# Kernel tuning notes

Hardware: AMD Instinct MI355X
Metric: run time of the kernel (lower is better)

## Reference

```python
import jax, jax.numpy as jnp
import numpy as np

N, E, DIN, DH, DE, DOUT, G = 100000, 1600000, 64, 128, 16, 1, 256

def setup_inputs() -> dict:
    key = jax.random.key(0)
    ks = jax.random.split(key, 16)
    p = lambda k, s: (jax.random.normal(k, s, dtype=jnp.float32) * 0.05)
    return {
        "x": jax.random.normal(ks[0], (N, DIN), dtype=jnp.float32),
        "edge_index": jax.random.randint(ks[1], (2, E), 0, N, dtype=jnp.int64),
        "edge_attr": jax.random.normal(ks[2], (E, DE), dtype=jnp.float32),
        "batch": jnp.sort(jax.random.randint(ks[3], (N,), 0, G, dtype=jnp.int64)),
        # GINEConv 1: edge lin (edge_dim -> input_dim) + mlp1 (DIN->DH->DH)
        "ew1": p(ks[4], (DIN, DE)), "eb1": p(ks[5], (DIN,)),
        "w1a": p(ks[6], (DH, DIN)), "b1a": p(ks[7], (DH,)),
        "w1b": p(ks[8], (DH, DH)), "b1b": p(ks[9], (DH,)),
        # GINEConv 2: edge lin (edge_dim -> hidden_dim) + mlp2 (DH->DH->DH)
        "ew2": p(ks[10], (DH, DE)), "eb2": p(ks[11], (DH,)),
        "w2a": p(ks[12], (DH, DH)), "b2a": p(ks[13], (DH,)),
        "w2b": p(ks[14], (DH, DH)), "b2b": p(ks[15], (DH,)),
        "wf": p(jax.random.fold_in(key, 99), (DOUT, DH)),
        "bf": jnp.zeros((DOUT,), dtype=jnp.float32),
    }

def _gine(x, src, dst, edge_attr, ew, eb, wa, ba, wb, bb):
    # message = relu(x[src] + Lin(edge_attr)); sum-aggregate at dst; eps=0
    msg = jax.nn.relu(x[src] + edge_attr @ ew.T + eb)          # [E, D]
    aggr = jax.ops.segment_sum(msg, dst, num_segments=x.shape[0])
    h = x + aggr                                               # (1+eps)*x + aggr, eps=0
    h = jax.nn.relu(h @ wa.T + ba)
    return h @ wb.T + bb

def reference(x, edge_index, edge_attr, batch, ew1, eb1, w1a, b1a, w1b, b1b,
              ew2, eb2, w2a, b2a, w2b, b2b, wf, bf):
    src, dst = edge_index[0], edge_index[1]
    h = _gine(x, src, dst, edge_attr, ew1, eb1, w1a, b1a, w1b, b1b)
    h = jax.nn.relu(h)  # dropout is identity in eval mode
    h = _gine(h, src, dst, edge_attr, ew2, eb2, w2a, b2a, w2b, b2b)
    h = jax.nn.relu(h)
    # global mean pool over graphs
    sums = jax.ops.segment_sum(h, batch, num_segments=G)       # [G, DH]
    cnts = jax.ops.segment_sum(jnp.ones((h.shape[0],), h.dtype), batch, num_segments=G)
    pooled = sums / jnp.maximum(cnts, 1.0)[:, None]
    return pooled @ wf.T + bf                                  # [G, DOUT]
```

## Files before the change

### kernel.cpp

```cpp
#include <hip/hip_runtime.h>

#define DINc 64
#define DHc  128
#define DEc  16
#define Gc   256
#define Rrep 64
#define SCB  1024

typedef unsigned short u16;
typedef unsigned int   u32;
typedef __attribute__((ext_vector_type(8))) short bf8;
typedef __attribute__((ext_vector_type(4))) short bf4;
typedef __attribute__((ext_vector_type(4))) float f4;

__device__ __forceinline__ u16 f2b(float f) {
  u32 u = __builtin_bit_cast(u32, f);
  u32 r = u + 0x7FFFu + ((u >> 16) & 1u);
  return (u16)(r >> 16);
}
__device__ __forceinline__ float b2f(u16 h) {
  u32 u = ((u32)h) << 16;
  return __builtin_bit_cast(float, u);
}

__global__ __launch_bounds__(256) void k_cvt(const float* __restrict__ x,
                                             u16* __restrict__ xb, const int n8) {
  for (int i = blockIdx.x * 256 + threadIdx.x; i < n8; i += gridDim.x * 256) {
    float4 f0 = *(const float4*)(x + (size_t)i * 8);
    float4 f1 = *(const float4*)(x + (size_t)i * 8 + 4);
    bf8 v;
    v[0]=(short)f2b(f0.x); v[1]=(short)f2b(f0.y); v[2]=(short)f2b(f0.z); v[3]=(short)f2b(f0.w);
    v[4]=(short)f2b(f1.x); v[5]=(short)f2b(f1.y); v[6]=(short)f2b(f1.z); v[7]=(short)f2b(f1.w);
    *(bf8*)(xb + (size_t)i * 8) = v;
  }
}

__global__ __launch_bounds__(256) void k_hist(const int* __restrict__ dstA, const int nE,
                                              int* __restrict__ deg) {
  for (int i = blockIdx.x * 256 + threadIdx.x; i < nE; i += gridDim.x * 256)
    atomicAdd(&deg[dstA[i]], 1);
}

__global__ __launch_bounds__(256) void k_scan_blk(const int* __restrict__ deg,
                                                  int* __restrict__ bsum, const int nN) {
  const int b = blockIdx.x, t = threadIdx.x;
  const int i0 = b * SCB + t * 4;
  int s = 0;
  #pragma unroll
  for (int q = 0; q < 4; ++q) { const int i = i0 + q; if (i < nN) s += deg[i]; }
  #pragma unroll
  for (int off = 32; off > 0; off >>= 1) s += __shfl_down(s, off);
  __shared__ int ws[4];
  if ((t & 63) == 0) ws[t >> 6] = s;
  __syncthreads();
  if (t == 0) bsum[b] = ws[0] + ws[1] + ws[2] + ws[3];
}

__global__ __launch_bounds__(256) void k_scan_fin(const int* __restrict__ deg,
                                                  const int* __restrict__ bsum,
                                                  int* __restrict__ rowptr,
                                                  const int nN, const int nB) {
  const int b = blockIdx.x, t = threadIdx.x;
  int p = 0;
  for (int i = t; i < b; i += 256) p += bsum[i];
  #pragma unroll
  for (int off = 32; off > 0; off >>= 1) p += __shfl_down(p, off);
  __shared__ int ws[4];
  __shared__ int sc[256];
  if ((t & 63) == 0) ws[t >> 6] = p;
  const int i0 = b * SCB + t * 4;
  int vals[4]; int s = 0;
  #pragma unroll
  for (int q = 0; q < 4; ++q) { const int i = i0 + q; vals[q] = (i < nN) ? deg[i] : 0; s += vals[q]; }
  sc[t] = s;
  __syncthreads();
  const int boff = ws[0] + ws[1] + ws[2] + ws[3];
  for (int off = 1; off < 256; off <<= 1) {
    int u = (t >= off) ? sc[t - off] : 0;
    __syncthreads();
    sc[t] += u;
    __syncthreads();
  }
  int run = boff + sc[t] - s;
  #pragma unroll
  for (int q = 0; q < 4; ++q) { const int i = i0 + q; if (i < nN) rowptr[i] = run; run += vals[q]; }
  if (b == nB - 1 && t == 255) rowptr[nN] = run;
}

__global__ __launch_bounds__(256) void k_fill(const int* __restrict__ dstA,
                                              const int* __restrict__ srcA, const int nE,
                                              const int* __restrict__ rowptr,
                                              int* __restrict__ cursor, int2* __restrict__ csr) {
  for (int i = blockIdx.x * 256 + threadIdx.x; i < nE; i += gridDim.x * 256) {
    const int d = dstA[i];
    const int pos = atomicAdd(&cursor[d], 1);
    csr[rowptr[d] + pos] = make_int2(i, srcA[i]);
  }
}

__global__ __launch_bounds__(256) void k_cnt_bs(const int* __restrict__ batch,
                                                float* __restrict__ cnts, const int nN) {
  const int g = threadIdx.x;
  if (g >= Gc) return;
  int lo = 0, hi = nN;
  while (lo < hi) { int m = (lo + hi) >> 1; if (batch[m] < g) lo = m + 1; else hi = m; }
  int lo2 = lo, hi2 = nN;
  while (lo2 < hi2) { int m = (lo2 + hi2) >> 1; if (batch[m] < g + 1) lo2 = m + 1; else hi2 = m; }
  cnts[g] = (float)(lo2 - lo);
}

template<int D>
__global__ __launch_bounds__(256) void gather_conv(
    const u16* __restrict__ xin, const int2* __restrict__ csr,
    const float* __restrict__ ea, const float* __restrict__ ew,
    const float* __restrict__ eb, const int* __restrict__ rowptr,
    float* __restrict__ aggr, const int nN)
{
  constexpr int PL = D / 64;
  __shared__ float eas[4][64][16];
  const int lane = threadIdx.x & 63;
  const int wv   = threadIdx.x >> 6;
  float (*E)[16] = eas[wv];
  float wreg[16 * PL];
  float ebr[PL];
  #pragma unroll
  for (int p = 0; p < PL; ++p) {
    const int d = lane * PL + p;
    ebr[p] = eb[d];
    #pragma unroll
    for (int k = 0; k < 16; ++k) wreg[k * PL + p] = ew[d * 16 + k];
  }
  const int wgid = blockIdx.x * 4 + wv;
  const int nw   = gridDim.x * 4;
  const int npw  = (nN + nw - 1) / nw;
  const int n0 = wgid * npw, n1 = min(n0 + npw, nN);
  for (int n = n0; n < n1; ++n) {
    const int beg = rowptr[n], end = rowptr[n + 1];
    float acc0 = 0.f, acc1 = 0.f;
    for (int chunk = beg; chunk < end; chunk += 64) {
      const int cnt = min(64, end - chunk);
      int2 es = (lane < cnt) ? csr[chunk + lane] : make_int2(0, 0);
      if (lane < cnt) {
        const float4* ep = (const float4*)(ea + (size_t)es.x * 16);
        float4 e0 = ep[0], e1 = ep[1], e2 = ep[2], e3 = ep[3];
        *(float4*)&E[lane][0]  = e0;
        *(float4*)&E[lane][4]  = e1;
        *(float4*)&E[lane][8]  = e2;
        *(float4*)&E[lane][12] = e3;
      }
      for (int i = 0; i < cnt; i += 8) {
        const int g = min(8, cnt - i);
        u32 xv[8];
        #pragma unroll
        for (int q = 0; q < 8; ++q) {
          if (q < g) {
            const int s = __builtin_amdgcn_readlane(es.y, i + q);
            if (PL == 1) xv[q] = (u32)xin[(size_t)s * 64 + lane];
            else         xv[q] = *(const u32*)(xin + (size_t)s * 128 + lane * 2);
          }
        }
        #pragma unroll
        for (int q = 0; q < 8; ++q) {
          if (q < g) {
            const float* Er = E[i + q];
            float ef[16];
            *(float4*)&ef[0]  = *(const float4*)(Er + 0);
            *(float4*)&ef[4]  = *(const float4*)(Er + 4);
            *(float4*)&ef[8]  = *(const float4*)(Er + 8);
            *(float4*)&ef[12] = *(const float4*)(Er + 12);
            if (PL == 1) {
              float v = ebr[0];
              #pragma unroll
              for (int k = 0; k < 16; ++k) v = fmaf(ef[k], wreg[k], v);
              acc0 += fmaxf(b2f((u16)xv[q]) + v, 0.f);
            } else {
              float v0 = ebr[0], v1 = ebr[1];
              #pragma unroll
              for (int k = 0; k < 16; ++k) {
                v0 = fmaf(ef[k], wreg[k * 2 + 0], v0);
                v1 = fmaf(ef[k], wreg[k * 2 + 1], v1);
              }
              acc0 += fmaxf(b2f((u16)(xv[q] & 0xFFFFu)) + v0, 0.f);
              acc1 += fmaxf(b2f((u16)(xv[q] >> 16)) + v1, 0.f);
            }
          }
        }
      }
    }
    if (PL == 1) aggr[(size_t)n * 64 + lane] = acc0;
    else *(float2*)(aggr + (size_t)n * 128 + lane * 2) = make_float2(acc0, acc1);
  }
}

template<int IN>
__global__ __launch_bounds__(256) void k_l1(
    const u16* __restrict__ xin, const float* __restrict__ aggr,
    const u16* __restrict__ waB, const float* __restrict__ ba,
    u16* __restrict__ tout, const int nN)
{
  __shared__ u16 wa_s[DHc * IN];
  __shared__ float ba_s[DHc];
  const int tid = threadIdx.x;
  constexpr int INC = IN / 8;
  for (int c = tid; c < DHc * INC; c += 256) {
    const int row = c / INC, kc = (c % INC) * 8;
    bf8 v = *(const bf8*)(waB + (size_t)row * IN + kc);
    *(bf8*)(wa_s + ((row * IN + kc) ^ ((row & 7) << 3))) = v;
  }
  if (tid < DHc) ba_s[tid] = ba[tid];
  __syncthreads();
  const int lane = tid & 63, wv = tid >> 6;
  const int lr = lane & 15, l4 = lane >> 4;
  const int nT = (nN + 15) >> 4;
  for (int tile = blockIdx.x * 4 + wv; tile < nT; tile += gridDim.x * 4) {
    const int node = tile * 16 + lr;
    const int n = min(node, nN - 1);
    bf8 bfr[IN / 32];
    #pragma unroll
    for (int ks = 0; ks < IN / 32; ++ks) {
      const int k0 = ks * 32 + l4 * 8;
      bf8 xv = *(const bf8*)(xin + (size_t)n * IN + k0);
      float4 a0 = *(const float4*)(aggr + (size_t)n * IN + k0);
      float4 a1 = *(const float4*)(aggr + (size_t)n * IN + k0 + 4);
      bf8 v;
      v[0] = (short)f2b(b2f((u16)xv[0]) + a0.x);
      v[1] = (short)f2b(b2f((u16)xv[1]) + a0.y);
      v[2] = (short)f2b(b2f((u16)xv[2]) + a0.z);
      v[3] = (short)f2b(b2f((u16)xv[3]) + a0.w);
      v[4] = (short)f2b(b2f((u16)xv[4]) + a1.x);
      v[5] = (short)f2b(b2f((u16)xv[5]) + a1.y);
      v[6] = (short)f2b(b2f((u16)xv[6]) + a1.z);
      v[7] = (short)f2b(b2f((u16)xv[7]) + a1.w);
      bfr[ks] = v;
    }
    const bool valid = node < nN;
    #pragma unroll
    for (int jt = 0; jt < 8; ++jt) {
      f4 c = {0.f, 0.f, 0.f, 0.f};
      #pragma unroll
      for (int ks = 0; ks < IN / 32; ++ks) {
        bf8 a = *(const bf8*)(wa_s + (((jt * 16 + lr) * IN + ks * 32 + l4 * 8) ^ ((lr & 7) << 3)));
        c = __builtin_amdgcn_mfma_f32_16x16x32_bf16(a, bfr[ks], c, 0, 0, 0);
      }
      if (valid) {
        float4 bav = *(const float4*)(ba_s + jt * 16 + l4 * 4);
        bf4 tv;
        tv[0] = (short)f2b(fmaxf(c[0] + bav.x, 0.f));
        tv[1] = (short)f2b(fmaxf(c[1] + bav.y, 0.f));
        tv[2] = (short)f2b(fmaxf(c[2] + bav.z, 0.f));
        tv[3] = (short)f2b(fmaxf(c[3] + bav.w, 0.f));
        *(bf4*)(tout + (size_t)node * DHc + jt * 16 + l4 * 4) = tv;
      }
    }
  }
}

template<bool FINAL>
__global__ __launch_bounds__(256) void k_l2(
    const u16* __restrict__ tin, const u16* __restrict__ wbB,
    const float* __restrict__ bb, u16* __restrict__ hout,
    const int* __restrict__ batch, float* __restrict__ sums, const int nN)
{
  __shared__ u16 wb_s[DHc * DHc];
  __shared__ float bb_s[DHc];
  const int tid = threadIdx.x;
  for (int c = tid; c < DHc * 16; c += 256) {
    const int row = c >> 4, kc = (c & 15) * 8;
    bf8 v = *(const bf8*)(wbB + (size_t)row * DHc + kc);
    *(bf8*)(wb_s + ((row * DHc + kc) ^ ((row & 7) << 3))) = v;
  }
  if (tid < DHc) bb_s[tid] = bb[tid];
  __syncthreads();
  const int lane = tid & 63, wv = tid >> 6;
  const int lr = lane & 15, l4 = lane >> 4;
  const int nT = (nN + 15) >> 4;
  const int gw0 = blockIdx.x * 4 + wv;
  const int rep = gw0 & (Rrep - 1);
  for (int tile = gw0; tile < nT; tile += gridDim.x * 4) {
    const int node0 = tile * 16;
    const int node = node0 + lr;
    const int n = min(node, nN - 1);
    bf8 tb[4];
    #pragma unroll
    for (int ks = 0; ks < 4; ++ks)
      tb[ks] = *(const bf8*)(tin + (size_t)n * DHc + ks * 32 + l4 * 8);
    const bool valid = node < nN;
    int gl = 0, g0 = 0; bool uni = false;
    if (FINAL) {
      gl = batch[n];
      g0 = __shfl(gl, 0);
      uni = __all(gl == g0) && (node0 + 16 <= nN);
    }
    #pragma unroll
    for (int jt = 0; jt < 8; ++jt) {
      f4 c = {0.f, 0.f, 0.f, 0.f};
      #pragma unroll
      for (int ks = 0; ks < 4; ++ks) {
        bf8 a = *(const bf8*)(wb_s + (((jt * 16 + lr) * DHc + ks * 32 + l4 * 8) ^ ((lr & 7) << 3)));
        c = __builtin_amdgcn_mfma_f32_16x16x32_bf16(a, tb[ks], c, 0, 0, 0);
      }
      float4 bbv = *(const float4*)(bb_s + jt * 16 + l4 * 4);
      float o0 = fmaxf(c[0] + bbv.x, 0.f);
      float o1 = fmaxf(c[1] + bbv.y, 0.f);
      float o2 = fmaxf(c[2] + bbv.z, 0.f);
      float o3 = fmaxf(c[3] + bbv.w, 0.f);
      if (!FINAL) {
        if (valid) {
          bf4 hv;
          hv[0] = (short)f2b(o0); hv[1] = (short)f2b(o1);
          hv[2] = (short)f2b(o2); hv[3] = (short)f2b(o3);
          *(bf4*)(hout + (size_t)node * DHc + jt * 16 + l4 * 4) = hv;
        }
      } else {
        if (uni) {
          #pragma unroll
          for (int off = 1; off < 16; off <<= 1) {
            o0 += __shfl_xor(o0, off);
            o1 += __shfl_xor(o1, off);
            o2 += __shfl_xor(o2, off);
            o3 += __shfl_xor(o3, off);
          }
          if (lr == 0) {
            float* dp = sums + ((size_t)rep * Gc + g0) * DHc + jt * 16 + l4 * 4;
            atomicAdd(dp + 0, o0); atomicAdd(dp + 1, o1);
            atomicAdd(dp + 2, o2); atomicAdd(dp + 3, o3);
          }
        } else if (valid) {
          float* dp = sums + ((size_t)rep * Gc + gl) * DHc + jt * 16 + l4 * 4;
          atomicAdd(dp + 0, o0); atomicAdd(dp + 1, o1);
          atomicAdd(dp + 2, o2); atomicAdd(dp + 3, o3);
        }
      }
    }
  }
}

__global__ __launch_bounds__(128) void pool_final(
    const float* __restrict__ sums, const float* __restrict__ cnts,
    const float* __restrict__ wf, const float* __restrict__ bf,
    float* __restrict__ out)
{
  const int g = blockIdx.x;
  const int j = threadIdx.x;
  float s = 0.f;
  for (int r = 0; r < Rrep; ++r) s += sums[((size_t)r * Gc + g) * DHc + j];
  const float ct = fmaxf(cnts[g], 1.f);
  __shared__ float red[128];
  red[j] = (s / ct) * wf[j];
  __syncthreads();
  for (int off = 64; off > 0; off >>= 1) { if (j < off) red[j] += red[j + off]; __syncthreads(); }
  if (j == 0) out[g] = red[0] + bf[0];
}

extern "C" void kernel_launch(void* const* d_in, const int* in_sizes, int n_in,
                              void* d_out, int out_size, void* d_ws, size_t ws_size,
                              hipStream_t stream) {
  const float* x    = (const float*)d_in[0];
  const int*   ei   = (const int*)d_in[1];
  const float* ea   = (const float*)d_in[2];
  const int*   batch= (const int*)d_in[3];
  const float* ew1  = (const float*)d_in[4];
  const float* eb1  = (const float*)d_in[5];
  const float* w1a  = (const float*)d_in[6];
  const float* b1a  = (const float*)d_in[7];
  const float* w1b  = (const float*)d_in[8];
  const float* b1b  = (const float*)d_in[9];
  const float* ew2  = (const float*)d_in[10];
  const float* eb2  = (const float*)d_in[11];
  const float* w2a  = (const float*)d_in[12];
  const float* b2a  = (const float*)d_in[13];
  const float* w2b  = (const float*)d_in[14];
  const float* b2b  = (const float*)d_in[15];
  const float* wf   = (const float*)d_in[16];
  const float* bf   = (const float*)d_in[17];
  float* out = (float*)d_out;

  const int nN = in_sizes[0] / DINc;
  const int nE = in_sizes[1] / 2;
  const int* srcA = ei;
  const int* dstA = ei + nE;

  char* wsb = (char*)d_ws;
  size_t o = 0;
  u16*   h1b    = (u16*)  (wsb + o); o += (size_t)nN * DHc * 2;
  u16*   xb     = (u16*)  (wsb + o); o += (size_t)nN * DINc * 2;
  u16*   tbuf   = (u16*)  (wsb + o); o += (size_t)nN * DHc * 2;
  float* aggr   = (float*)(wsb + o); o += (size_t)nN * DHc * 4;
  float* sums   = (float*)(wsb + o); o += (size_t)Rrep * Gc * DHc * 4;
  float* cnts   = (float*)(wsb + o); o += (size_t)Gc * 4;
  int*   deg    = (int*)  (wsb + o); o += (size_t)nN * 4;
  int*   cursor = (int*)  (wsb + o); o += (size_t)nN * 4;
  int*   rowptr = (int*)  (wsb + o); o += (size_t)(nN + 1) * 4;
  int*   bsum   = (int*)  (wsb + o); o += (size_t)((nN + SCB - 1) / SCB) * 4; o = (o + 15) & ~(size_t)15;
  int2*  csr    = (int2*) (wsb + o); o += (size_t)nE * 8;
  u16*   w1ab   = (u16*)  (wsb + o); o += (size_t)DHc * DINc * 2;
  u16*   w1bb   = (u16*)  (wsb + o); o += (size_t)DHc * DHc * 2;
  u16*   w2ab   = (u16*)  (wsb + o); o += (size_t)DHc * DHc * 2;
  u16*   w2bb   = (u16*)  (wsb + o); o += (size_t)DHc * DHc * 2;
  (void)ws_size; (void)n_in; (void)out_size;

  hipMemsetAsync(sums, 0, (size_t)Rrep * Gc * DHc * 4 + (size_t)Gc * 4, stream);
  hipMemsetAsync(deg, 0, (size_t)nN * 8, stream);

  const int nB = (nN + SCB - 1) / SCB;
  k_cvt<<<1024, 256, 0, stream>>>(x, xb, nN * DINc / 8);
  k_cvt<<<4, 256, 0, stream>>>(w1a, w1ab, DHc * DINc / 8);
  k_cvt<<<8, 256, 0, stream>>>(w1b, w1bb, DHc * DHc / 8);
  k_cvt<<<8, 256, 0, stream>>>(w2a, w2ab, DHc * DHc / 8);
  k_cvt<<<8, 256, 0, stream>>>(w2b, w2bb, DHc * DHc / 8);
  k_hist<<<1024, 256, 0, stream>>>(dstA, nE, deg);
  k_scan_blk<<<nB, 256, 0, stream>>>(deg, bsum, nN);
  k_scan_fin<<<nB, 256, 0, stream>>>(deg, bsum, rowptr, nN, nB);
  k_fill<<<1024, 256, 0, stream>>>(dstA, srcA, nE, rowptr, cursor, csr);
  k_cnt_bs<<<1, 256, 0, stream>>>(batch, cnts, nN);

  const int nT = (nN + 15) / 16;
  const int mg = (nT + 3) / 4;
  gather_conv<DINc><<<2048, 256, 0, stream>>>(xb, csr, ea, ew1, eb1, rowptr, aggr, nN);
  k_l1<DINc><<<mg, 256, 0, stream>>>(xb, aggr, w1ab, b1a, tbuf, nN);
  k_l2<false><<<mg, 256, 0, stream>>>(tbuf, w1bb, b1b, h1b, nullptr, nullptr, nN);
  gather_conv<DHc><<<2048, 256, 0, stream>>>(h1b, csr, ea, ew2, eb2, rowptr, aggr, nN);
  k_l1<DHc><<<mg, 256, 0, stream>>>(h1b, aggr, w2ab, b2a, tbuf, nN);
  k_l2<true><<<mg, 256, 0, stream>>>(tbuf, w2bb, b2b, nullptr, batch, sums, nN);
  pool_final<<<Gc, 128, 0, stream>>>(sums, cnts, wf, bf, out);
}
```

Before: 577.9 us.

## Compute edge linear with MFMA and process edges in flat per-wave ranges

```diff
diff --git a/kernel.cpp b/kernel.cpp
--- a/kernel.cpp
+++ b/kernel.cpp
@@ -1,4 +1,5 @@
 #include <hip/hip_runtime.h>
+#include <hip/hip_bf16.h>
 
 #define DINc 64
 #define DHc  128
@@ -12,6 +13,7 @@
 typedef __attribute__((ext_vector_type(8))) short bf8;
 typedef __attribute__((ext_vector_type(4))) short bf4;
 typedef __attribute__((ext_vector_type(4))) float f4;
+typedef __attribute__((ext_vector_type(4))) unsigned int u32x4;
 
 __device__ __forceinline__ u16 f2b(float f) {
   u32 u = __builtin_bit_cast(u32, f);
@@ -21,6 +23,9 @@
 __device__ __forceinline__ float b2f(u16 h) {
   u32 u = ((u32)h) << 16;
   return __builtin_bit_cast(float, u);
+}
+__device__ __forceinline__ u32 pkbf(float a, float b) {
+  return ((u32)f2b(b) << 16) | (u32)f2b(a);
 }
 
 __global__ __launch_bounds__(256) void k_cvt(const float* __restrict__ x,
@@ -90,11 +95,13 @@
 __global__ __launch_bounds__(256) void k_fill(const int* __restrict__ dstA,
                                               const int* __restrict__ srcA, const int nE,
                                               const int* __restrict__ rowptr,
-                                              int* __restrict__ cursor, int2* __restrict__ csr) {
+                                              int* __restrict__ cursor, int2* __restrict__ csr,
+                                              int* __restrict__ dstC) {
   for (int i = blockIdx.x * 256 + threadIdx.x; i < nE; i += gridDim.x * 256) {
     const int d = dstA[i];
     const int pos = atomicAdd(&cursor[d], 1);
     csr[rowptr[d] + pos] = make_int2(i, srcA[i]);
+    dstC[rowptr[d] + pos] = d;
   }
 }
 
@@ -110,85 +117,135 @@
 }
 
 template<int D>
-__global__ __launch_bounds__(256) void gather_conv(
+__global__ __launch_bounds__(256) void gather_mfma(
     const u16* __restrict__ xin, const int2* __restrict__ csr,
-    const float* __restrict__ ea, const float* __restrict__ ew,
-    const float* __restrict__ eb, const int* __restrict__ rowptr,
-    float* __restrict__ aggr, const int nN)
+    const int* __restrict__ dstC, const float* __restrict__ ea,
+    const float* __restrict__ ewg, const float* __restrict__ ebg,
+    const int* __restrict__ rowptr, float* __restrict__ aggr, const int nN)
 {
-  constexpr int PL = D / 64;
-  __shared__ float eas[4][64][16];
-  const int lane = threadIdx.x & 63;
-  const int wv   = threadIdx.x >> 6;
-  float (*E)[16] = eas[wv];
-  float wreg[16 * PL];
-  float ebr[PL];
-  #pragma unroll
-  for (int p = 0; p < PL; ++p) {
-    const int d = lane * PL + p;
-    ebr[p] = eb[d];
-    #pragma unroll
-    for (int k = 0; k < 16; ++k) wreg[k * PL + p] = ew[d * 16 + k];
-  }
+  constexpr int NT = D / 16;
+  __shared__ u16 elin[4][D][66];
+  const int lane = threadIdx.x & 63, wv = threadIdx.x >> 6;
+  const int lr = lane & 15, l4 = lane >> 4;
+  u16 (*E)[66] = elin[wv];
+
+  bf8 ewf[NT]; float ebr[NT];
+  #pragma unroll
+  for (int nt = 0; nt < NT; ++nt) {
+    const int d = nt * 16 + lr;
+    ebr[nt] = ebg[d];
+    u32x4 w = {0u, 0u, 0u, 0u};
+    if (l4 < 2) {
+      f4 a0 = *(const f4*)(ewg + d * 16 + l4 * 8);
+      f4 a1 = *(const f4*)(ewg + d * 16 + l4 * 8 + 4);
+      w[0] = pkbf(a0[0], a0[1]); w[1] = pkbf(a0[2], a0[3]);
+      w[2] = pkbf(a1[0], a1[1]); w[3] = pkbf(a1[2], a1[3]);
+    }
+    ewf[nt] = __builtin_bit_cast(bf8, w);
+  }
+
   const int wgid = blockIdx.x * 4 + wv;
   const int nw   = gridDim.x * 4;
   const int npw  = (nN + nw - 1) / nw;
-  const int n0 = wgid * npw, n1 = min(n0 + npw, nN);
-  for (int n = n0; n < n1; ++n) {
-    const int beg = rowptr[n], end = rowptr[n + 1];
-    float acc0 = 0.f, acc1 = 0.f;
-    for (int chunk = beg; chunk < end; chunk += 64) {
-      const int cnt = min(64, end - chunk);
-      int2 es = (lane < cnt) ? csr[chunk + lane] : make_int2(0, 0);
-      if (lane < cnt) {
-        const float4* ep = (const float4*)(ea + (size_t)es.x * 16);
-        float4 e0 = ep[0], e1 = ep[1], e2 = ep[2], e3 = ep[3];
-        *(float4*)&E[lane][0]  = e0;
-        *(float4*)&E[lane][4]  = e1;
-        *(float4*)&E[lane][8]  = e2;
-        *(float4*)&E[lane][12] = e3;
-      }
-      for (int i = 0; i < cnt; i += 8) {
-        const int g = min(8, cnt - i);
-        u32 xv[8];
-        #pragma unroll
-        for (int q = 0; q < 8; ++q) {
-          if (q < g) {
-            const int s = __builtin_amdgcn_readlane(es.y, i + q);
-            if (PL == 1) xv[q] = (u32)xin[(size_t)s * 64 + lane];
-            else         xv[q] = *(const u32*)(xin + (size_t)s * 128 + lane * 2);
+  const int n0 = min(wgid * npw, nN), n1 = min(n0 + npw, nN);
+  if (n0 >= n1) return;
+  const int e0 = rowptr[n0], e1 = rowptr[n1];
+
+  float acc0 = 0.f, acc1 = 0.f;
+  int cur = n0 - 1;
+
+  for (int chunk = e0; chunk < e1; chunk += 64) {
+    const int cnt = min(64, e1 - chunk);
+    int2 es = (lane < cnt) ? csr[chunk + lane] : make_int2(0, 0);
+    int dl  = (lane < cnt) ? dstC[chunk + lane] : -1;
+    const int pd = __shfl_up(dl, 1);
+    const bool bnd = (lane < cnt) && (dl != ((lane == 0) ? cur : pd));
+    const unsigned long long bmask = __ballot(bnd);
+
+    const int nmt = (cnt + 15) >> 4;
+    for (int mt = 0; mt < nmt; ++mt) {
+      const int eix = __shfl(es.x, mt * 16 + lr);
+      u32x4 aw = {0u, 0u, 0u, 0u};
+      if (l4 < 2) {
+        f4 a0 = *(const f4*)(ea + (size_t)eix * 16 + l4 * 8);
+        f4 a1 = *(const f4*)(ea + (size_t)eix * 16 + l4 * 8 + 4);
+        aw[0] = pkbf(a0[0], a0[1]); aw[1] = pkbf(a0[2], a0[3]);
+        aw[2] = pkbf(a1[0], a1[1]); aw[3] = pkbf(a1[2], a1[3]);
+      }
+      const bf8 af = __builtin_bit_cast(bf8, aw);
+      #pragma unroll
+      for (int nt = 0; nt < NT; ++nt) {
+        f4 c = {0.f, 0.f, 0.f, 0.f};
+        c = __builtin_amdgcn_mfma_f32_16x16x32_bf16(af, ewf[nt], c, 0, 0, 0);
+        const u32 lo = pkbf(c[0] + ebr[nt], c[1] + ebr[nt]);
+        const u32 hi = pkbf(c[2] + ebr[nt], c[3] + ebr[nt]);
+        u32* dp = (u32*)&E[nt * 16 + lr][mt * 16 + l4 * 4];
+        dp[0] = lo; dp[1] = hi;
+      }
+    }
+
+    for (int i = 0; i < cnt; i += 8) {
+      const int g = min(8, cnt - i);
+      u32 xv[8];
+      #pragma unroll
+      for (int q = 0; q < 8; ++q) {
+        if (q < g) {
+          const int s = __builtin_amdgcn_readlane(es.y, i + q);
+          if (D == 128) xv[q] = *(const u32*)(xin + (size_t)s * 128 + lane * 2);
+          else          xv[q] = (u32)xin[(size_t)s * 64 + lane];
+        }
+      }
+      u32 ra[4], rb[4];
+      #pragma unroll
+      for (int pp = 0; pp < 4; ++pp) {
+        if (pp * 2 < g) {
+          if (D == 128) {
+            ra[pp] = *(const u32*)&E[lane * 2    ][i + pp * 2];
+            rb[pp] = *(const u32*)&E[lane * 2 + 1][i + pp * 2];
+          } else {
+            ra[pp] = *(const u32*)&E[lane][i + pp * 2];
           }
         }
-        #pragma unroll
-        for (int q = 0; q < 8; ++q) {
-          if (q < g) {
-            const float* Er = E[i + q];
-            float ef[16];
-            *(float4*)&ef[0]  = *(const float4*)(Er + 0);
-            *(float4*)&ef[4]  = *(const float4*)(Er + 4);
-            *(float4*)&ef[8]  = *(const float4*)(Er + 8);
-            *(float4*)&ef[12] = *(const float4*)(Er + 12);
-            if (PL == 1) {
-              float v = ebr[0];
-              #pragma unroll
-              for (int k = 0; k < 16; ++k) v = fmaf(ef[k], wreg[k], v);
-              acc0 += fmaxf(b2f((u16)xv[q]) + v, 0.f);
-            } else {
-              float v0 = ebr[0], v1 = ebr[1];
-              #pragma unroll
-              for (int k = 0; k < 16; ++k) {
-                v0 = fmaf(ef[k], wreg[k * 2 + 0], v0);
-                v1 = fmaf(ef[k], wreg[k * 2 + 1], v1);
-              }
-              acc0 += fmaxf(b2f((u16)(xv[q] & 0xFFFFu)) + v0, 0.f);
-              acc1 += fmaxf(b2f((u16)(xv[q] >> 16)) + v1, 0.f);
+      }
+      #pragma unroll
+      for (int q = 0; q < 8; ++q) {
+        if (q < g) {
+          const int e = i + q;
+          if ((bmask >> e) & 1ull) {
+            const int nd = __builtin_amdgcn_readlane(dl, e);
+            if (cur >= n0) {
+              if (D == 128) *(float2*)(aggr + (size_t)cur * 128 + lane * 2) = make_float2(acc0, acc1);
+              else          aggr[(size_t)cur * 64 + lane] = acc0;
             }
+            for (int m = cur + 1; m < nd; ++m) {
+              if (D == 128) *(float2*)(aggr + (size_t)m * 128 + lane * 2) = make_float2(0.f, 0.f);
+              else          aggr[(size_t)m * 64 + lane] = 0.f;
+            }
+            acc0 = 0.f; acc1 = 0.f;
+            cur = nd;
+          }
+          if (D == 128) {
+            const u32 wa_ = ra[q >> 1], wb_ = rb[q >> 1];
+            const float ev0 = b2f((u16)((q & 1) ? (wa_ >> 16) : (wa_ & 0xFFFFu)));
+            const float ev1 = b2f((u16)((q & 1) ? (wb_ >> 16) : (wb_ & 0xFFFFu)));
+            acc0 += fmaxf(b2f((u16)(xv[q] & 0xFFFFu)) + ev0, 0.f);
+            acc1 += fmaxf(b2f((u16)(xv[q] >> 16)) + ev1, 0.f);
+          } else {
+            const u32 wa_ = ra[q >> 1];
+            const float ev = b2f((u16)((q & 1) ? (wa_ >> 16) : (wa_ & 0xFFFFu)));
+            acc0 += fmaxf(b2f((u16)xv[q]) + ev, 0.f);
           }
         }
       }
     }
-    if (PL == 1) aggr[(size_t)n * 64 + lane] = acc0;
-    else *(float2*)(aggr + (size_t)n * 128 + lane * 2) = make_float2(acc0, acc1);
+  }
+  if (cur >= n0) {
+    if (D == 128) *(float2*)(aggr + (size_t)cur * 128 + lane * 2) = make_float2(acc0, acc1);
+    else          aggr[(size_t)cur * 64 + lane] = acc0;
+  }
+  for (int m = cur + 1; m < n1; ++m) {
+    if (D == 128) *(float2*)(aggr + (size_t)m * 128 + lane * 2) = make_float2(0.f, 0.f);
+    else          aggr[(size_t)m * 64 + lane] = 0.f;
   }
 }
 
@@ -393,6 +450,7 @@
   int*   rowptr = (int*)  (wsb + o); o += (size_t)(nN + 1) * 4;
   int*   bsum   = (int*)  (wsb + o); o += (size_t)((nN + SCB - 1) / SCB) * 4; o = (o + 15) & ~(size_t)15;
   int2*  csr    = (int2*) (wsb + o); o += (size_t)nE * 8;
+  int*   dstC   = (int*)  (wsb + o); o += (size_t)nE * 4;
   u16*   w1ab   = (u16*)  (wsb + o); o += (size_t)DHc * DINc * 2;
   u16*   w1bb   = (u16*)  (wsb + o); o += (size_t)DHc * DHc * 2;
   u16*   w2ab   = (u16*)  (wsb + o); o += (size_t)DHc * DHc * 2;
@@ -411,15 +469,15 @@
   k_hist<<<1024, 256, 0, stream>>>(dstA, nE, deg);
   k_scan_blk<<<nB, 256, 0, stream>>>(deg, bsum, nN);
   k_scan_fin<<<nB, 256, 0, stream>>>(deg, bsum, rowptr, nN, nB);
-  k_fill<<<1024, 256, 0, stream>>>(dstA, srcA, nE, rowptr, cursor, csr);
+  k_fill<<<1024, 256, 0, stream>>>(dstA, srcA, nE, rowptr, cursor, csr, dstC);
   k_cnt_bs<<<1, 256, 0, stream>>>(batch, cnts, nN);
 
   const int nT = (nN + 15) / 16;
   const int mg = (nT + 3) / 4;
-  gather_conv<DINc><<<2048, 256, 0, stream>>>(xb, csr, ea, ew1, eb1, rowptr, aggr, nN);
+  gather_mfma<DINc><<<2048, 256, 0, stream>>>(xb, csr, dstC, ea, ew1, eb1, rowptr, aggr, nN);
   k_l1<DINc><<<mg, 256, 0, stream>>>(xb, aggr, w1ab, b1a, tbuf, nN);
   k_l2<false><<<mg, 256, 0, stream>>>(tbuf, w1bb, b1b, h1b, nullptr, nullptr, nN);
-  gather_conv<DHc><<<2048, 256, 0, stream>>>(h1b, csr, ea, ew2, eb2, rowptr, aggr, nN);
+  gather_mfma<DHc><<<2048, 256, 0, stream>>>(h1b, csr, dstC, ea, ew2, eb2, rowptr, aggr, nN);
   k_l1<DHc><<<mg, 256, 0, stream>>>(h1b, aggr, w2ab, b2a, tbuf, nN);
   k_l2<true><<<mg, 256, 0, stream>>>(tbuf, w2bb, b2b, nullptr, batch, sums, nN);
   pool_final<<<Gc, 128, 0, stream>>>(sums, cnts, wf, bf, out);
```

Measured after the change: 689.0 us. +19.2%, slower.
